# Kernel optimization log

Measured on AMD Instinct MI355X. Metric: run time of the kernel, lower is better.

Reference implementation:

```python
import jax, jax.numpy as jnp
import numpy as np

B, C, H, W = 8, 512, 64, 64
NUMS, V_C = 1024, 512
RATE = 0.999


def _normalize(x):
    # matches torch F.normalize(dim=-1, eps=1e-12)
    return x / jnp.clip(jnp.linalg.norm(x, axis=-1, keepdims=True), 1e-12)


def setup_inputs() -> dict:
    key = jax.random.key(0)
    k1, k2, k3 = jax.random.split(key, 3)
    return {
        "x": jax.random.normal(k1, (B, C, H, W), dtype=jnp.float32),
        "noise_feature": jax.random.normal(k2, (NUMS, C), dtype=jnp.float32),
        "std": jax.random.normal(k3, (NUMS, V_C), dtype=jnp.float32),
    }


def reference(x, noise_feature, std):
    b, c, h, w = x.shape
    # (b,c,h,w) -> (n,c)
    xf = jnp.transpose(x, (0, 2, 3, 1)).reshape(-1, c)
    m = jax.lax.stop_gradient(noise_feature)  # torch uses .data (no grad)
    xn = _normalize(xf)
    mn = _normalize(m)
    score = xn @ mn.T  # (n, k) cosine similarities

    # EMA codebook update (training path, update_flag=True)
    xd = jax.lax.stop_gradient(xf)
    embed_ind = jnp.argmax(score, axis=1)  # (n,)
    # segment_sum == x.T @ one_hot(ind), transposed; avoids dense one-hot GEMM
    embed_sum = jax.ops.segment_sum(xd, embed_ind, num_segments=NUMS)  # (k, c)
    counts = jax.ops.segment_sum(jnp.ones((xd.shape[0],), xd.dtype), embed_ind,
                                 num_segments=NUMS)  # (k,)
    embed_mean = embed_sum / (counts[:, None] + 1e-6)
    new_m = m * RATE + embed_mean * (1.0 - RATE)

    mn2 = _normalize(new_m)
    score2 = xn @ mn2.T  # (n, k)
    soft_label = jax.nn.softmax(score2, axis=1)
    out = (soft_label @ std).reshape(b, h, w, V_C)
    return out, score2
```

## Files before the change

### kernel.cpp

```cpp
#include <hip/hip_runtime.h>
#include <stdint.h>

#define NROWS 32768
#define CDIM  512
#define KCODES 1024
#define VC    512
#define LDP 72

typedef unsigned short u16;
typedef unsigned long long u64;
using bf16x8 = __attribute__((ext_vector_type(8))) __bf16;
using f32x4  = __attribute__((ext_vector_type(4))) float;

__device__ __forceinline__ float bf2f(u16 u){
  union { unsigned int i; float f; } x; x.i = ((unsigned int)u) << 16; return x.f;
}
__device__ __forceinline__ u16 f2bf(float f){
  union { float f; unsigned int i; } x; x.f = f;
  unsigned int u = x.i;
  u += 0x7fffu + ((u >> 16) & 1u);
  return (u16)(u >> 16);
}
__device__ __forceinline__ unsigned int pack2(u16 lo, u16 hi){
  return (unsigned int)lo | ((unsigned int)hi << 16);
}
__device__ __forceinline__ unsigned int fkey(float f){
  unsigned int u = __float_as_uint(f);
  return (u & 0x80000000u) ? ~u : (u | 0x80000000u);
}
__device__ __forceinline__ f32x4 mfma16(bf16x8 a, bf16x8 b, f32x4 c){
  return __builtin_amdgcn_mfma_f32_16x16x32_bf16(a, b, c, 0, 0, 0);
}

__global__ __launch_bounds__(256) void k_transpose_x(const float* __restrict__ x,
                                                     u16* __restrict__ xf){
  __shared__ float tile[32][33];
  int b  = blockIdx.z;
  int p0 = blockIdx.x * 32;
  int c0 = blockIdx.y * 32;
  int tx = threadIdx.x, ty = threadIdx.y;
  const float* xb = x + (size_t)b * CDIM * 4096;
#pragma unroll
  for (int i = 0; i < 4; i++){
    int c = c0 + ty + i * 8;
    tile[ty + i * 8][tx] = xb[(size_t)c * 4096 + p0 + tx];
  }
  __syncthreads();
#pragma unroll
  for (int i = 0; i < 4; i++){
    int p = p0 + ty + i * 8;
    xf[((size_t)(b * 4096 + p)) * CDIM + c0 + tx] = f2bf(tile[tx][ty + i * 8]);
  }
}

__global__ __launch_bounds__(256) void k_rownorm(const u16* __restrict__ xf,
                                                 float* __restrict__ rinv){
  int row  = blockIdx.x * 4 + (threadIdx.x >> 6);
  int lane = threadIdx.x & 63;
  const uint4* p = (const uint4*)(xf + (size_t)row * CDIM);
  uint4 v = p[lane];
  unsigned int w[4] = {v.x, v.y, v.z, v.w};
  float s = 0.f;
#pragma unroll
  for (int i = 0; i < 4; i++){
    float a = bf2f((u16)(w[i] & 0xffffu));
    float b = bf2f((u16)(w[i] >> 16));
    s += a * a + b * b;
  }
#pragma unroll
  for (int off = 32; off; off >>= 1) s += __shfl_xor(s, off, 64);
  if (lane == 0) rinv[row] = 1.0f / fmaxf(sqrtf(s), 1e-12f);
}

__global__ __launch_bounds__(256) void k_norm_rows(const float* __restrict__ in,
                                                   u16* __restrict__ out){
  int row  = blockIdx.x * 4 + (threadIdx.x >> 6);
  int lane = threadIdx.x & 63;
  const float* r = in + (size_t)row * CDIM;
  float v[8]; float s = 0.f;
#pragma unroll
  for (int i = 0; i < 8; i++){ v[i] = r[lane + i * 64]; s += v[i] * v[i]; }
#pragma unroll
  for (int off = 32; off; off >>= 1) s += __shfl_xor(s, off, 64);
  float inv = 1.0f / fmaxf(sqrtf(s), 1e-12f);
#pragma unroll
  for (int i = 0; i < 8; i++) out[(size_t)row * CDIM + lane + i * 64] = f2bf(v[i] * inv);
}

__global__ __launch_bounds__(256) void k_transpose_std(const float* __restrict__ sd,
                                                       u16* __restrict__ stdT){
  __shared__ float tile[32][33];
  int k0 = blockIdx.x * 32;
  int v0 = blockIdx.y * 32;
  int tx = threadIdx.x, ty = threadIdx.y;
#pragma unroll
  for (int i = 0; i < 4; i++)
    tile[ty + i * 8][tx] = sd[(size_t)(k0 + ty + i * 8) * VC + v0 + tx];
  __syncthreads();
#pragma unroll
  for (int i = 0; i < 4; i++)
    stdT[(size_t)(v0 + ty + i * 8) * KCODES + k0 + tx] = f2bf(tile[tx][ty + i * 8]);
}

__global__ __launch_bounds__(256) void k_gemm1_am(const u16* __restrict__ xf,
                                                  const u16* __restrict__ mn,
                                                  u64* __restrict__ packed){
  __shared__ u16 As[128 * LDP];
  __shared__ u16 Bs[128 * LDP];
  int tid  = threadIdx.x;
  int wave = tid >> 6, lane = tid & 63;
  int wr = wave >> 1, wc = wave & 1;
  int quad = lane >> 4, l15 = lane & 15;
  int c0 = blockIdx.x * 128, r0 = blockIdx.y * 128;
  int row = tid >> 1, half = tid & 1;

  f32x4 acc[4][4];
#pragma unroll
  for (int rt = 0; rt < 4; rt++)
#pragma unroll
    for (int ct = 0; ct < 4; ct++) acc[rt][ct] = (f32x4)(0.f);

  const u16* ag = xf + (size_t)(r0 + row) * CDIM + half * 32;
  const u16* bg = mn + (size_t)(c0 + row) * CDIM + half * 32;

  for (int k0 = 0; k0 < CDIM; k0 += 64){
    const uint4* asrc = (const uint4*)(ag + k0);
    const uint4* bsrc = (const uint4*)(bg + k0);
    uint4* adst = (uint4*)(As + row * LDP + half * 32);
    uint4* bdst = (uint4*)(Bs + row * LDP + half * 32);
#pragma unroll
    for (int j = 0; j < 4; j++){ adst[j] = asrc[j]; bdst[j] = bsrc[j]; }
    __syncthreads();
#pragma unroll
    for (int ks = 0; ks < 2; ks++){
      bf16x8 af[4], bf[4];
#pragma unroll
      for (int rt = 0; rt < 4; rt++)
        af[rt] = *(const bf16x8*)(As + (wr * 64 + rt * 16 + l15) * LDP + ks * 32 + quad * 8);
#pragma unroll
      for (int ct = 0; ct < 4; ct++)
        bf[ct] = *(const bf16x8*)(Bs + (wc * 64 + ct * 16 + l15) * LDP + ks * 32 + quad * 8);
#pragma unroll
      for (int rt = 0; rt < 4; rt++)
#pragma unroll
        for (int ct = 0; ct < 4; ct++)
          acc[rt][ct] = mfma16(af[rt], bf[ct], acc[rt][ct]);
    }
    __syncthreads();
  }

#pragma unroll
  for (int rt = 0; rt < 4; rt++){
#pragma unroll
    for (int q = 0; q < 4; q++){
      float bv = acc[rt][0][q];
      int   bc = c0 + wc * 64 + l15;
#pragma unroll
      for (int ct = 1; ct < 4; ct++){
        float v = acc[rt][ct][q];
        int   c = c0 + wc * 64 + ct * 16 + l15;
        if (v > bv){ bv = v; bc = c; }
      }
#pragma unroll
      for (int off = 1; off <= 8; off <<= 1){
        float ov = __shfl_xor(bv, off, 64);
        int   oc = __shfl_xor(bc, off, 64);
        if (ov > bv || (ov == bv && oc < bc)){ bv = ov; bc = oc; }
      }
      if (l15 == 0){
        int rg = r0 + wr * 64 + rt * 16 + quad * 4 + q;
        u64 key = ((u64)fkey(bv) << 32) | (unsigned int)(~(unsigned int)bc);
        atomicMax(packed + rg, key);
      }
    }
  }
}

__global__ __launch_bounds__(256) void k_decode(const u64* __restrict__ packed,
                                                int* __restrict__ ind){
  int i = blockIdx.x * 256 + threadIdx.x;
  ind[i] = (int)(~(unsigned int)(packed[i] & 0xffffffffull)) & (KCODES - 1);
}

__global__ __launch_bounds__(256) void k_gather(const int* __restrict__ ind,
                                                const u16* __restrict__ xf,
                                                float* __restrict__ esum,
                                                float* __restrict__ counts){
  __shared__ float part[4][CDIM];
  __shared__ int   wcnt[4];
  int code = blockIdx.x;
  int tid = threadIdx.x, wave = tid >> 6, lane = tid & 63;
  float acc[8] = {0,0,0,0,0,0,0,0};
  int cnt = 0;
  for (int base = wave * 64; base < NROWS; base += 256){
    int match = (ind[base + lane] == code);
    u64 mask = __ballot(match);
    cnt += (int)__popcll(mask);
    while (mask){
      int b = __ffsll((long long)mask) - 1;
      mask &= mask - 1;
      int rr = base + b;
      uint4 v = *(const uint4*)(xf + (size_t)rr * CDIM + lane * 8);
      unsigned int w[4] = {v.x, v.y, v.z, v.w};
#pragma unroll
      for (int i = 0; i < 4; i++){
        acc[2 * i]     += bf2f((u16)(w[i] & 0xffffu));
        acc[2 * i + 1] += bf2f((u16)(w[i] >> 16));
      }
    }
  }
#pragma unroll
  for (int j = 0; j < 8; j++) part[wave][lane * 8 + j] = acc[j];
  if (lane == 0) wcnt[wave] = cnt;
  __syncthreads();
  for (int c = tid; c < CDIM; c += 256)
    esum[(size_t)code * CDIM + c] = part[0][c] + part[1][c] + part[2][c] + part[3][c];
  if (tid == 0) counts[code] = (float)(wcnt[0] + wcnt[1] + wcnt[2] + wcnt[3]);
}

__global__ __launch_bounds__(256) void k_newm(const float* __restrict__ m,
                                              const float* __restrict__ esum,
                                              const float* __restrict__ counts,
                                              u16* __restrict__ mn2){
  int row  = blockIdx.x * 4 + (threadIdx.x >> 6);
  int lane = threadIdx.x & 63;
  float cnt = counts[row];
  float sc  = 0.001f / (cnt + 1e-6f);
  float v[8]; float s = 0.f;
#pragma unroll
  for (int i = 0; i < 8; i++){
    int c = lane + i * 64;
    v[i] = m[(size_t)row * CDIM + c] * 0.999f + esum[(size_t)row * CDIM + c] * sc;
    s += v[i] * v[i];
  }
#pragma unroll
  for (int off = 32; off; off >>= 1) s += __shfl_xor(s, off, 64);
  float inv = 1.0f / fmaxf(sqrtf(s), 1e-12f);
#pragma unroll
  for (int i = 0; i < 8; i++) mn2[(size_t)row * CDIM + lane + i * 64] = f2bf(v[i] * inv);
}

__global__ __launch_bounds__(256) void k_gemm2(const u16* __restrict__ xf,
                                               const u16* __restrict__ mn2,
                                               const float* __restrict__ rinv,
                                               float* __restrict__ score2){
  __shared__ u16 As[128 * LDP];
  __shared__ u16 Bs[128 * LDP];
  int tid  = threadIdx.x;
  int wave = tid >> 6, lane = tid & 63;
  int wr = wave >> 1, wc = wave & 1;
  int quad = lane >> 4, l15 = lane & 15;
  int c0 = blockIdx.x * 128, r0 = blockIdx.y * 128;
  int row = tid >> 1, half = tid & 1;

  f32x4 acc[4][4];
#pragma unroll
  for (int rt = 0; rt < 4; rt++)
#pragma unroll
    for (int ct = 0; ct < 4; ct++) acc[rt][ct] = (f32x4)(0.f);

  const u16* ag = xf  + (size_t)(r0 + row) * CDIM + half * 32;
  const u16* bg = mn2 + (size_t)(c0 + row) * CDIM + half * 32;

  for (int k0 = 0; k0 < CDIM; k0 += 64){
    const uint4* asrc = (const uint4*)(ag + k0);
    const uint4* bsrc = (const uint4*)(bg + k0);
    uint4* adst = (uint4*)(As + row * LDP + half * 32);
    uint4* bdst = (uint4*)(Bs + row * LDP + half * 32);
#pragma unroll
    for (int j = 0; j < 4; j++){ adst[j] = asrc[j]; bdst[j] = bsrc[j]; }
    __syncthreads();
#pragma unroll
    for (int ks = 0; ks < 2; ks++){
      bf16x8 af[4], bf[4];
#pragma unroll
      for (int rt = 0; rt < 4; rt++)
        af[rt] = *(const bf16x8*)(As + (wr * 64 + rt * 16 + l15) * LDP + ks * 32 + quad * 8);
#pragma unroll
      for (int ct = 0; ct < 4; ct++)
        bf[ct] = *(const bf16x8*)(Bs + (wc * 64 + ct * 16 + l15) * LDP + ks * 32 + quad * 8);
#pragma unroll
      for (int rt = 0; rt < 4; rt++)
#pragma unroll
        for (int ct = 0; ct < 4; ct++)
          acc[rt][ct] = mfma16(af[rt], bf[ct], acc[rt][ct]);
    }
    __syncthreads();
  }
#pragma unroll
  for (int rt = 0; rt < 4; rt++){
#pragma unroll
    for (int q = 0; q < 4; q++){
      int grow = r0 + wr * 64 + rt * 16 + quad * 4 + q;
      float rv = rinv[grow];
#pragma unroll
      for (int ct = 0; ct < 4; ct++){
        int gcol = c0 + wc * 64 + ct * 16 + l15;
        score2[(size_t)grow * KCODES + gcol] = acc[rt][ct][q] * rv;
      }
    }
  }
}

__global__ __launch_bounds__(256) void k_softstats(const float* __restrict__ score2,
                                                   float* __restrict__ rowmax,
                                                   float* __restrict__ rsinv){
  int row = blockIdx.x, tid = threadIdx.x;
  int wave = tid >> 6, lane = tid & 63;
  float4 v = ((const float4*)(score2 + (size_t)row * KCODES))[tid];
  float mx = fmaxf(fmaxf(v.x, v.y), fmaxf(v.z, v.w));
#pragma unroll
  for (int off = 32; off; off >>= 1) mx = fmaxf(mx, __shfl_xor(mx, off, 64));
  __shared__ float red[4], red2[4];
  if (lane == 0) red[wave] = mx;
  __syncthreads();
  mx = fmaxf(fmaxf(red[0], red[1]), fmaxf(red[2], red[3]));
  float s = __expf(v.x - mx) + __expf(v.y - mx) + __expf(v.z - mx) + __expf(v.w - mx);
#pragma unroll
  for (int off = 32; off; off >>= 1) s += __shfl_xor(s, off, 64);
  if (lane == 0) red2[wave] = s;
  __syncthreads();
  if (tid == 0){ rowmax[row] = mx; rsinv[row] = 1.0f / (red2[0] + red2[1] + red2[2] + red2[3]); }
}

__global__ __launch_bounds__(512) void k_gemm3(const float* __restrict__ score2,
                                               const float* __restrict__ rowmax,
                                               const float* __restrict__ rsinv,
                                               const u16* __restrict__ stdT,
                                               float* __restrict__ out){
  __shared__ u16 As[128 * LDP];
  __shared__ u16 Bs[256 * LDP];
  int tid  = threadIdx.x;
  int wave = tid >> 6, lane = tid & 63;
  int wr = wave >> 2, wcol = wave & 3;
  int quad = lane >> 4, l15 = lane & 15;
  int c0 = blockIdx.x * 256, r0 = blockIdx.y * 128;
  int arow = tid >> 2, aq = tid & 3;
  int brow = tid >> 1, bhalf = tid & 1;

  float rmax = rowmax[r0 + arow];
  float rs   = rsinv [r0 + arow];

  f32x4 acc[4][4];
#pragma unroll
  for (int rt = 0; rt < 4; rt++)
#pragma unroll
    for (int ct = 0; ct < 4; ct++) acc[rt][ct] = (f32x4)(0.f);

  const float* ag = score2 + (size_t)(r0 + arow) * KCODES + aq * 16;
  const u16*   bg = stdT   + (size_t)(c0 + brow) * KCODES + bhalf * 32;

  for (int k0 = 0; k0 < KCODES; k0 += 64){
#pragma unroll
    for (int j = 0; j < 2; j++){
      float4 a = *(const float4*)(ag + k0 + j * 8);
      float4 b = *(const float4*)(ag + k0 + j * 8 + 4);
      uint4 o;
      o.x = pack2(f2bf(__expf(a.x - rmax) * rs), f2bf(__expf(a.y - rmax) * rs));
      o.y = pack2(f2bf(__expf(a.z - rmax) * rs), f2bf(__expf(a.w - rmax) * rs));
      o.z = pack2(f2bf(__expf(b.x - rmax) * rs), f2bf(__expf(b.y - rmax) * rs));
      o.w = pack2(f2bf(__expf(b.z - rmax) * rs), f2bf(__expf(b.w - rmax) * rs));
      *(uint4*)(As + arow * LDP + aq * 16 + j * 8) = o;
    }
#pragma unroll
    for (int j = 0; j < 4; j++)
      *(uint4*)(Bs + brow * LDP + bhalf * 32 + j * 8) =
          *(const uint4*)(bg + k0 + j * 8);
    __syncthreads();
#pragma unroll
    for (int ks = 0; ks < 2; ks++){
      bf16x8 af[4], bf[4];
#pragma unroll
      for (int rt = 0; rt < 4; rt++)
        af[rt] = *(const bf16x8*)(As + (wr * 64 + rt * 16 + l15) * LDP + ks * 32 + quad * 8);
#pragma unroll
      for (int ct = 0; ct < 4; ct++)
        bf[ct] = *(const bf16x8*)(Bs + (wcol * 64 + ct * 16 + l15) * LDP + ks * 32 + quad * 8);
#pragma unroll
      for (int rt = 0; rt < 4; rt++)
#pragma unroll
        for (int ct = 0; ct < 4; ct++)
          acc[rt][ct] = mfma16(af[rt], bf[ct], acc[rt][ct]);
    }
    __syncthreads();
  }
#pragma unroll
  for (int rt = 0; rt < 4; rt++){
#pragma unroll
    for (int q = 0; q < 4; q++){
      int grow = r0 + wr * 64 + rt * 16 + quad * 4 + q;
#pragma unroll
      for (int ct = 0; ct < 4; ct++){
        int gcol = c0 + wcol * 64 + ct * 16 + l15;
        out[(size_t)grow * VC + gcol] = acc[rt][ct][q];
      }
    }
  }
}

extern "C" void kernel_launch(void* const* d_in, const int* in_sizes, int n_in,
                              void* d_out, int out_size, void* d_ws, size_t ws_size,
                              hipStream_t stream){
  (void)in_sizes; (void)n_in; (void)out_size; (void)ws_size;
  const float* x      = (const float*)d_in[0];
  const float* m      = (const float*)d_in[1];
  const float* stdmat = (const float*)d_in[2];
  float* out    = (float*)d_out;
  float* score2 = out + (size_t)NROWS * VC;

  char* ws = (char*)d_ws;
  u16*   xf     = (u16*)  (ws + 0);
  u16*   mn     = (u16*)  (ws + 33554432);
  u16*   mn2    = (u16*)  (ws + 34603008);
  u16*   stdT   = (u16*)  (ws + 35651584);
  float* rinv   = (float*)(ws + 36700160);
  u64*   packed = (u64*)  (ws + 36831232);
  int*   ind    = (int*)  (ws + 37093376);
  float* esum   = (float*)(ws + 37224448);
  float* counts = (float*)(ws + 39321600);
  float* rowmax = (float*)(ws + 39325696);
  float* rsinv  = (float*)(ws + 39456768);

  hipMemsetAsync(packed, 0, (size_t)NROWS * 8, stream);

  k_transpose_x  <<<dim3(128, 16, 8), dim3(32, 8), 0, stream>>>(x, xf);
  k_rownorm      <<<NROWS / 4, 256, 0, stream>>>(xf, rinv);
  k_norm_rows    <<<KCODES / 4, 256, 0, stream>>>(m, mn);
  k_transpose_std<<<dim3(32, 16), dim3(32, 8), 0, stream>>>(stdmat, stdT);
  k_gemm1_am     <<<dim3(KCODES / 128, NROWS / 128), 256, 0, stream>>>(xf, mn, packed);
  k_decode       <<<NROWS / 256, 256, 0, stream>>>(packed, ind);
  k_gather       <<<KCODES, 256, 0, stream>>>(ind, xf, esum, counts);
  k_newm         <<<KCODES / 4, 256, 0, stream>>>(m, esum, counts, mn2);
  k_gemm2        <<<dim3(KCODES / 128, NROWS / 128), 256, 0, stream>>>(xf, mn2, rinv, score2);
  k_softstats    <<<NROWS, 256, 0, stream>>>(score2, rowmax, rsinv);
  k_gemm3        <<<dim3(VC / 256, NROWS / 128), 512, 0, stream>>>(score2, rowmax, rsinv, stdT, out);
}
```

Measured before the change: 508.3 us.

## Use direct global-to-LDS loads in GEMMs and fuse softmax stats into GEMM2

```diff
diff --git a/kernel.cpp b/kernel.cpp
--- a/kernel.cpp
+++ b/kernel.cpp
@@ -30,6 +30,11 @@
 }
 __device__ __forceinline__ f32x4 mfma16(bf16x8 a, bf16x8 b, f32x4 c){
   return __builtin_amdgcn_mfma_f32_16x16x32_bf16(a, b, c, 0, 0, 0);
+}
+__device__ __forceinline__ void gload_lds16(const void* g, void* l){
+  __builtin_amdgcn_global_load_lds(
+      (const __attribute__((address_space(1))) unsigned int*)g,
+      (__attribute__((address_space(3))) unsigned int*)l, 16, 0, 0);
 }
 
 __global__ __launch_bounds__(256) void k_transpose_x(const float* __restrict__ x,
@@ -105,14 +110,19 @@
 __global__ __launch_bounds__(256) void k_gemm1_am(const u16* __restrict__ xf,
                                                   const u16* __restrict__ mn,
                                                   u64* __restrict__ packed){
-  __shared__ u16 As[128 * LDP];
-  __shared__ u16 Bs[128 * LDP];
+  __shared__ u16 As[128 * 64];
+  __shared__ u16 Bs[128 * 64];
   int tid  = threadIdx.x;
   int wave = tid >> 6, lane = tid & 63;
   int wr = wave >> 1, wc = wave & 1;
   int quad = lane >> 4, l15 = lane & 15;
   int c0 = blockIdx.x * 128, r0 = blockIdx.y * 128;
-  int row = tid >> 1, half = tid & 1;
+
+  int srow = lane >> 3, schunk = lane & 7;
+  const u16* ag = xf + (size_t)(r0 + wave * 8 + srow) * CDIM + schunk * 8;
+  const u16* bg = mn + (size_t)(c0 + wave * 8 + srow) * CDIM + schunk * 8;
+  u16* adst = As + wave * 8 * 64;
+  u16* bdst = Bs + wave * 8 * 64;
 
   f32x4 acc[4][4];
 #pragma unroll
@@ -120,31 +130,27 @@
 #pragma unroll
     for (int ct = 0; ct < 4; ct++) acc[rt][ct] = (f32x4)(0.f);
 
-  const u16* ag = xf + (size_t)(r0 + row) * CDIM + half * 32;
-  const u16* bg = mn + (size_t)(c0 + row) * CDIM + half * 32;
-
   for (int k0 = 0; k0 < CDIM; k0 += 64){
-    const uint4* asrc = (const uint4*)(ag + k0);
-    const uint4* bsrc = (const uint4*)(bg + k0);
-    uint4* adst = (uint4*)(As + row * LDP + half * 32);
-    uint4* bdst = (uint4*)(Bs + row * LDP + half * 32);
-#pragma unroll
-    for (int j = 0; j < 4; j++){ adst[j] = asrc[j]; bdst[j] = bsrc[j]; }
+#pragma unroll
+    for (int i = 0; i < 4; i++){
+      gload_lds16(ag + (size_t)i * 32 * CDIM + k0, adst + i * 32 * 64);
+      gload_lds16(bg + (size_t)i * 32 * CDIM + k0, bdst + i * 32 * 64);
+    }
     __syncthreads();
 #pragma unroll
     for (int ks = 0; ks < 2; ks++){
-      bf16x8 af[4], bf[4];
-#pragma unroll
-      for (int rt = 0; rt < 4; rt++)
-        af[rt] = *(const bf16x8*)(As + (wr * 64 + rt * 16 + l15) * LDP + ks * 32 + quad * 8);
+      bf16x8 af[4], bfr[4];
+#pragma unroll
+      for (int rt = 0; rt < 4; rt++)
+        af[rt] = *(const bf16x8*)(As + (wr * 64 + rt * 16 + l15) * 64 + ks * 32 + quad * 8);
 #pragma unroll
       for (int ct = 0; ct < 4; ct++)
-        bf[ct] = *(const bf16x8*)(Bs + (wc * 64 + ct * 16 + l15) * LDP + ks * 32 + quad * 8);
+        bfr[ct] = *(const bf16x8*)(Bs + (wc * 64 + ct * 16 + l15) * 64 + ks * 32 + quad * 8);
 #pragma unroll
       for (int rt = 0; rt < 4; rt++)
 #pragma unroll
         for (int ct = 0; ct < 4; ct++)
-          acc[rt][ct] = mfma16(af[rt], bf[ct], acc[rt][ct]);
+          acc[rt][ct] = mfma16(af[rt], bfr[ct], acc[rt][ct]);
     }
     __syncthreads();
   }
@@ -243,15 +249,22 @@
 __global__ __launch_bounds__(256) void k_gemm2(const u16* __restrict__ xf,
                                                const u16* __restrict__ mn2,
                                                const float* __restrict__ rinv,
-                                               float* __restrict__ score2){
-  __shared__ u16 As[128 * LDP];
-  __shared__ u16 Bs[128 * LDP];
+                                               float* __restrict__ score2,
+                                               float* __restrict__ pmax,
+                                               float* __restrict__ psum){
+  __shared__ u16 As[128 * 64];
+  __shared__ u16 Bs[128 * 64];
   int tid  = threadIdx.x;
   int wave = tid >> 6, lane = tid & 63;
   int wr = wave >> 1, wc = wave & 1;
   int quad = lane >> 4, l15 = lane & 15;
   int c0 = blockIdx.x * 128, r0 = blockIdx.y * 128;
-  int row = tid >> 1, half = tid & 1;
+
+  int srow = lane >> 3, schunk = lane & 7;
+  const u16* ag = xf  + (size_t)(r0 + wave * 8 + srow) * CDIM + schunk * 8;
+  const u16* bg = mn2 + (size_t)(c0 + wave * 8 + srow) * CDIM + schunk * 8;
+  u16* adst = As + wave * 8 * 64;
+  u16* bdst = Bs + wave * 8 * 64;
 
   f32x4 acc[4][4];
 #pragma unroll
@@ -259,68 +272,76 @@
 #pragma unroll
     for (int ct = 0; ct < 4; ct++) acc[rt][ct] = (f32x4)(0.f);
 
-  const u16* ag = xf  + (size_t)(r0 + row) * CDIM + half * 32;
-  const u16* bg = mn2 + (size_t)(c0 + row) * CDIM + half * 32;
-
   for (int k0 = 0; k0 < CDIM; k0 += 64){
-    const uint4* asrc = (const uint4*)(ag + k0);
-    const uint4* bsrc = (const uint4*)(bg + k0);
-    uint4* adst = (uint4*)(As + row * LDP + half * 32);
-    uint4* bdst = (uint4*)(Bs + row * LDP + half * 32);
-#pragma unroll
-    for (int j = 0; j < 4; j++){ adst[j] = asrc[j]; bdst[j] = bsrc[j]; }
+#pragma unroll
+    for (int i = 0; i < 4; i++){
+      gload_lds16(ag + (size_t)i * 32 * CDIM + k0, adst + i * 32 * 64);
+      gload_lds16(bg + (size_t)i * 32 * CDIM + k0, bdst + i * 32 * 64);
+    }
     __syncthreads();
 #pragma unroll
     for (int ks = 0; ks < 2; ks++){
-      bf16x8 af[4], bf[4];
-#pragma unroll
-      for (int rt = 0; rt < 4; rt++)
-        af[rt] = *(const bf16x8*)(As + (wr * 64 + rt * 16 + l15) * LDP + ks * 32 + quad * 8);
+      bf16x8 af[4], bfr[4];
+#pragma unroll
+      for (int rt = 0; rt < 4; rt++)
+        af[rt] = *(const bf16x8*)(As + (wr * 64 + rt * 16 + l15) * 64 + ks * 32 + quad * 8);
 #pragma unroll
       for (int ct = 0; ct < 4; ct++)
-        bf[ct] = *(const bf16x8*)(Bs + (wc * 64 + ct * 16 + l15) * LDP + ks * 32 + quad * 8);
+        bfr[ct] = *(const bf16x8*)(Bs + (wc * 64 + ct * 16 + l15) * 64 + ks * 32 + quad * 8);
 #pragma unroll
       for (int rt = 0; rt < 4; rt++)
 #pragma unroll
         for (int ct = 0; ct < 4; ct++)
-          acc[rt][ct] = mfma16(af[rt], bf[ct], acc[rt][ct]);
-    }
-    __syncthreads();
-  }
+          acc[rt][ct] = mfma16(af[rt], bfr[ct], acc[rt][ct]);
+    }
+    __syncthreads();
+  }
+
 #pragma unroll
   for (int rt = 0; rt < 4; rt++){
 #pragma unroll
     for (int q = 0; q < 4; q++){
       int grow = r0 + wr * 64 + rt * 16 + quad * 4 + q;
       float rv = rinv[grow];
-#pragma unroll
-      for (int ct = 0; ct < 4; ct++){
-        int gcol = c0 + wc * 64 + ct * 16 + l15;
-        score2[(size_t)grow * KCODES + gcol] = acc[rt][ct][q] * rv;
-      }
-    }
-  }
-}
-
-__global__ __launch_bounds__(256) void k_softstats(const float* __restrict__ score2,
-                                                   float* __restrict__ rowmax,
-                                                   float* __restrict__ rsinv){
-  int row = blockIdx.x, tid = threadIdx.x;
-  int wave = tid >> 6, lane = tid & 63;
-  float4 v = ((const float4*)(score2 + (size_t)row * KCODES))[tid];
-  float mx = fmaxf(fmaxf(v.x, v.y), fmaxf(v.z, v.w));
-#pragma unroll
-  for (int off = 32; off; off >>= 1) mx = fmaxf(mx, __shfl_xor(mx, off, 64));
-  __shared__ float red[4], red2[4];
-  if (lane == 0) red[wave] = mx;
-  __syncthreads();
-  mx = fmaxf(fmaxf(red[0], red[1]), fmaxf(red[2], red[3]));
-  float s = __expf(v.x - mx) + __expf(v.y - mx) + __expf(v.z - mx) + __expf(v.w - mx);
-#pragma unroll
-  for (int off = 32; off; off >>= 1) s += __shfl_xor(s, off, 64);
-  if (lane == 0) red2[wave] = s;
-  __syncthreads();
-  if (tid == 0){ rowmax[row] = mx; rsinv[row] = 1.0f / (red2[0] + red2[1] + red2[2] + red2[3]); }
+      float v0 = acc[rt][0][q] * rv;
+      float v1 = acc[rt][1][q] * rv;
+      float v2 = acc[rt][2][q] * rv;
+      float v3 = acc[rt][3][q] * rv;
+      float* so = score2 + (size_t)grow * KCODES + c0 + wc * 64 + l15;
+      so[0]  = v0;
+      so[16] = v1;
+      so[32] = v2;
+      so[48] = v3;
+      float mx = fmaxf(fmaxf(v0, v1), fmaxf(v2, v3));
+#pragma unroll
+      for (int off = 1; off <= 8; off <<= 1) mx = fmaxf(mx, __shfl_xor(mx, off, 64));
+      float s = __expf(v0 - mx) + __expf(v1 - mx) + __expf(v2 - mx) + __expf(v3 - mx);
+#pragma unroll
+      for (int off = 1; off <= 8; off <<= 1) s += __shfl_xor(s, off, 64);
+      if (l15 == 0){
+        int pi = grow * 16 + blockIdx.x * 2 + wc;
+        pmax[pi] = mx;
+        psum[pi] = s;
+      }
+    }
+  }
+}
+
+__global__ __launch_bounds__(256) void k_softcomb(const float* __restrict__ pmax,
+                                                  const float* __restrict__ psum,
+                                                  float* __restrict__ rowmax,
+                                                  float* __restrict__ rsinv){
+  int row = blockIdx.x * 256 + threadIdx.x;
+  const float* pm = pmax + (size_t)row * 16;
+  const float* ps = psum + (size_t)row * 16;
+  float M = pm[0];
+#pragma unroll
+  for (int i = 1; i < 16; i++) M = fmaxf(M, pm[i]);
+  float S = 0.f;
+#pragma unroll
+  for (int i = 0; i < 16; i++) S += ps[i] * __expf(pm[i] - M);
+  rowmax[row] = M;
+  rsinv[row]  = 1.0f / S;
 }
 
 __global__ __launch_bounds__(512) void k_gemm3(const float* __restrict__ score2,
@@ -329,14 +350,17 @@
                                                const u16* __restrict__ stdT,
                                                float* __restrict__ out){
   __shared__ u16 As[128 * LDP];
-  __shared__ u16 Bs[256 * LDP];
+  __shared__ u16 Bs[256 * 64];
   int tid  = threadIdx.x;
   int wave = tid >> 6, lane = tid & 63;
   int wr = wave >> 2, wcol = wave & 3;
   int quad = lane >> 4, l15 = lane & 15;
   int c0 = blockIdx.x * 256, r0 = blockIdx.y * 128;
   int arow = tid >> 2, aq = tid & 3;
-  int brow = tid >> 1, bhalf = tid & 1;
+
+  int srow = lane >> 3, schunk = lane & 7;
+  const u16* bg = stdT + (size_t)(c0 + wave * 8 + srow) * KCODES + schunk * 8;
+  u16* bdst = Bs + wave * 8 * 64;
 
   float rmax = rowmax[r0 + arow];
   float rs   = rsinv [r0 + arow];
@@ -348,9 +372,11 @@
     for (int ct = 0; ct < 4; ct++) acc[rt][ct] = (f32x4)(0.f);
 
   const float* ag = score2 + (size_t)(r0 + arow) * KCODES + aq * 16;
-  const u16*   bg = stdT   + (size_t)(c0 + brow) * KCODES + bhalf * 32;
 
   for (int k0 = 0; k0 < KCODES; k0 += 64){
+#pragma unroll
+    for (int i = 0; i < 4; i++)
+      gload_lds16(bg + (size_t)i * 64 * KCODES + k0, bdst + i * 64 * 64);
 #pragma unroll
     for (int j = 0; j < 2; j++){
       float4 a = *(const float4*)(ag + k0 + j * 8);
@@ -362,25 +388,21 @@
       o.w = pack2(f2bf(__expf(b.z - rmax) * rs), f2bf(__expf(b.w - rmax) * rs));
       *(uint4*)(As + arow * LDP + aq * 16 + j * 8) = o;
     }
-#pragma unroll
-    for (int j = 0; j < 4; j++)
-      *(uint4*)(Bs + brow * LDP + bhalf * 32 + j * 8) =
-          *(const uint4*)(bg + k0 + j * 8);
     __syncthreads();
 #pragma unroll
     for (int ks = 0; ks < 2; ks++){
-      bf16x8 af[4], bf[4];
+      bf16x8 af[4], bfr[4];
 #pragma unroll
       for (int rt = 0; rt < 4; rt++)
         af[rt] = *(const bf16x8*)(As + (wr * 64 + rt * 16 + l15) * LDP + ks * 32 + quad * 8);
 #pragma unroll
       for (int ct = 0; ct < 4; ct++)
-        bf[ct] = *(const bf16x8*)(Bs + (wcol * 64 + ct * 16 + l15) * LDP + ks * 32 + quad * 8);
+        bfr[ct] = *(const bf16x8*)(Bs + (wcol * 64 + ct * 16 + l15) * 64 + ks * 32 + quad * 8);
 #pragma unroll
       for (int rt = 0; rt < 4; rt++)
 #pragma unroll
         for (int ct = 0; ct < 4; ct++)
-          acc[rt][ct] = mfma16(af[rt], bf[ct], acc[rt][ct]);
+          acc[rt][ct] = mfma16(af[rt], bfr[ct], acc[rt][ct]);
     }
     __syncthreads();
   }
@@ -420,6 +442,8 @@
   float* counts = (float*)(ws + 39321600);
   float* rowmax = (float*)(ws + 39325696);
   float* rsinv  = (float*)(ws + 39456768);
+  float* pmax   = (float*)(ws + 39587840);
+  float* psum   = (float*)(ws + 41684992);
 
   hipMemsetAsync(packed, 0, (size_t)NROWS * 8, stream);
 
@@ -431,7 +455,7 @@
   k_decode       <<<NROWS / 256, 256, 0, stream>>>(packed, ind);
   k_gather       <<<KCODES, 256, 0, stream>>>(ind, xf, esum, counts);
   k_newm         <<<KCODES / 4, 256, 0, stream>>>(m, esum, counts, mn2);
-  k_gemm2        <<<dim3(KCODES / 128, NROWS / 128), 256, 0, stream>>>(xf, mn2, rinv, score2);
-  k_softstats    <<<NROWS, 256, 0, stream>>>(score2, rowmax, rsinv);
+  k_gemm2        <<<dim3(KCODES / 128, NROWS / 128), 256, 0, stream>>>(xf, mn2, rinv, score2, pmax, psum);
+  k_softcomb     <<<NROWS / 256, 256, 0, stream>>>(pmax, psum, rowmax, rsinv);
   k_gemm3        <<<dim3(VC / 256, NROWS / 128), 512, 0, stream>>>(score2, rowmax, rsinv, stdT, out);
 }
```

Result: no change. 507.2 us (-0.2%).
